# Optimization experiments

Measured on AMD Instinct MI355X. Metric: run time of the kernel, lower is better.

## Reference

```python
import jax, jax.numpy as jnp
import numpy as np
from jax import lax

B, L = 32, 128
WORD_DIM, TAG_DIM = 300, 100
EMB = WORD_DIM + TAG_DIM  # 400; LSTM hidden size == EMB
H = EMB
WV, TV = 30000, 50
MLP_H = 100


def _mk(k, shape):
    return jax.random.normal(k, shape, dtype=jnp.float32) * 0.05


def setup_inputs():
    key = jax.random.key(0)
    ks = iter(jax.random.split(key, 40))
    d = {}
    d["words_idx_tensor"] = jax.random.randint(next(ks), (B, L), 0, WV)
    d["tags_idx_tensor"] = jax.random.randint(next(ks), (B, L), 0, TV)
    d["max_length"] = L
    d["lengths"] = jax.random.randint(next(ks), (B,), 1, L + 1)
    d["word_emb"] = _mk(next(ks), (WV, WORD_DIM))
    d["tag_emb"] = _mk(next(ks), (TV, TAG_DIM))
    for name, din in (("l0", EMB), ("l0r", EMB), ("l1", 2 * H), ("l1r", 2 * H)):
        d["w_ih_" + name] = _mk(next(ks), (4 * H, din))
        d["w_hh_" + name] = _mk(next(ks), (4 * H, H))
        d["b_ih_" + name] = _mk(next(ks), (4 * H,))
        d["b_hh_" + name] = _mk(next(ks), (4 * H,))
    d["w1"] = _mk(next(ks), (MLP_H, 4 * H))
    d["b1"] = _mk(next(ks), (MLP_H,))
    d["w2"] = _mk(next(ks), (1, MLP_H))
    d["b2"] = _mk(next(ks), (1,))
    return d


def _lstm_dir(x, w_ih, w_hh, b_ih, b_hh, reverse):
    # x: (T, N, Din) time-major. PyTorch gate order: i, f, g, o.
    T, N, _ = x.shape
    xg = jnp.einsum('tnd,gd->tng', x, w_ih) + b_ih + b_hh  # (T, N, 4H)

    def step(carry, g_in):
        h, c = carry
        g = g_in + h @ w_hh.T
        i, f, gg, o = jnp.split(g, 4, axis=-1)
        c = jax.nn.sigmoid(f) * c + jax.nn.sigmoid(i) * jnp.tanh(gg)
        h = jax.nn.sigmoid(o) * jnp.tanh(c)
        return (h, c), h

    init = (jnp.zeros((N, H), x.dtype), jnp.zeros((N, H), x.dtype))
    _, hs = lax.scan(step, init, xg, reverse=reverse)
    return hs  # (T, N, H) in original time order (matches PyTorch bidir)


def _forward(words_idx, tags_idx, max_length, p):
    we = p["word_emb"][words_idx[:, :max_length]]   # (B, L, 300)
    te = p["tag_emb"][tags_idx[:, :max_length]]     # (B, L, 100)
    embeds = jnp.concatenate([we, te], axis=2)       # (B, L, 400)
    # Faithful to `embeds.view(L, B, -1)`: a RESHAPE, not a transpose.
    x = embeds.reshape(max_length, embeds.shape[0], -1)  # (L, B, 400)
    # batch_first LSTM sees batch=L, seq=B -> time-major over axis B
    h = jnp.swapaxes(x, 0, 1)                        # (B, L, 400)
    for layer in ("l0", "l1"):
        hf = _lstm_dir(h, p["w_ih_" + layer], p["w_hh_" + layer],
                       p["b_ih_" + layer], p["b_hh_" + layer], False)
        hb = _lstm_dir(h, p["w_ih_" + layer + "r"], p["w_hh_" + layer + "r"],
                       p["b_ih_" + layer + "r"], p["b_hh_" + layer + "r"], True)
        h = jnp.concatenate([hf, hb], axis=-1)       # (B, L, 2H)
    lstm_out = jnp.swapaxes(h, 0, 1)                 # (L, B, 2H)
    # Pairwise concat + Linear factorized: W1 @ [h_i; h_j] = W1a h_i + W1b h_j
    w1a, w1b = p["w1"][:, :2 * H], p["w1"][:, 2 * H:]
    a = jnp.einsum('lbd,hd->lbh', lstm_out, w1a)     # (L, B, 100)
    bm = jnp.einsum('lbd,hd->lbh', lstm_out, w1b) + p["b1"]
    hid = jnp.tanh(a[:, None] + bm[None, :])         # (L, L, B, 100)
    out = jnp.einsum('ijbh,oh->ijbo', hid, p["w2"]) + p["b2"]  # (L, L, B, 1)
    # matches torch.stack order: feature index = i * L + j
    return out.reshape(max_length * max_length, lstm_out.shape[1], 1)


def reference(words_idx_tensor, tags_idx_tensor, max_length, lengths,
              word_emb, tag_emb,
              w_ih_l0, w_hh_l0, b_ih_l0, b_hh_l0,
              w_ih_l0r, w_hh_l0r, b_ih_l0r, b_hh_l0r,
              w_ih_l1, w_hh_l1, b_ih_l1, b_hh_l1,
              w_ih_l1r, w_hh_l1r, b_ih_l1r, b_hh_l1r,
              w1, b1, w2, b2):
    p = dict(locals())
    return _forward(words_idx_tensor, tags_idx_tensor, max_length, p)
```

## Files before the change

### kernel.cpp

```cpp
#include <hip/hip_runtime.h>

typedef unsigned short u16;
typedef unsigned int u32;
typedef __attribute__((ext_vector_type(8))) short bf16x8;
typedef __attribute__((ext_vector_type(4))) float f32x4;

#define TSEQ 32
#define NB   128
#define HDIM 400
#define KPAD 416
#define G4   1600
#define TOK  4096
#define XGC  3200
#define BPITCH 420

__device__ __forceinline__ float b2f(u16 u) {
  union { unsigned int i; float f; } v; v.i = ((unsigned int)u) << 16; return v.f;
}
__device__ __forceinline__ u16 f2b(float f) {
  union { float fl; unsigned int i; } v; v.fl = f;
  unsigned int r = v.i + 0x7fffu + ((v.i >> 16) & 1u);
  return (u16)(r >> 16);
}
__device__ __forceinline__ float loadf(const void* p, long long i, int isbf) {
  return isbf ? b2f(((const u16*)p)[i]) : ((const float*)p)[i];
}
__device__ __forceinline__ u16 loadb(const void* p, long long i, int isbf) {
  return isbf ? ((const u16*)p)[i] : f2b(((const float*)p)[i]);
}
__device__ __forceinline__ float sigm_(float x) { return 1.0f / (1.0f + __expf(-x)); }
__device__ __forceinline__ float tanh_(float x) {
  float e = __expf(2.0f * x);
  return 1.0f - 2.0f / (e + 1.0f);
}

__device__ __forceinline__ void store_h16(u16* p, unsigned v) {
  asm volatile("global_store_short %0, %1, off sc0 sc1" :: "v"(p), "v"(v) : "memory");
}
__device__ __forceinline__ void store_flag(unsigned* p, unsigned v) {
  asm volatile("global_store_dword %0, %1, off sc0 sc1" :: "v"(p), "v"(v) : "memory");
}
__device__ __forceinline__ unsigned poll_cnt(const unsigned* p) {
  unsigned v;
  asm volatile("global_load_dword %0, %1, off sc0 sc1\n\ts_waitcnt vmcnt(0)"
               : "=v"(v) : "v"(p) : "memory");
  return v;
}

__global__ __launch_bounds__(256) void sniff_kernel(const void* wemb, int* flag) {
  __shared__ int cf, cb;
  if (threadIdx.x == 0) { cf = 0; cb = 0; }
  __syncthreads();
  int okf = 0, okb = 0;
  for (int i = threadIdx.x; i < 8192; i += 256) {
    float f = ((const float*)wemb)[i];
    float af = fabsf(f);
    if (af > 1e-12f && af < 8.0f) okf++;
    u16 ub = ((const u16*)wemb)[i];
    float fb = b2f(ub); float ab = fabsf(fb);
    if (ub == 0 || (ab > 1e-12f && ab < 8.0f)) okb++;
  }
  atomicAdd(&cf, okf);
  atomicAdd(&cb, okb);
  __syncthreads();
  if (threadIdx.x == 0) flag[0] = (cb > cf) ? 1 : 0;
}

__global__ __launch_bounds__(256) void embed_kernel(
    const int* __restrict__ words, const int* __restrict__ tags,
    const void* __restrict__ wemb, const void* __restrict__ temb,
    const int* __restrict__ flag, u16* __restrict__ XP) {
  const int isbf = flag[0];
  int idx = blockIdx.x * 256 + threadIdx.x;
  if (idx >= TOK * 400) return;
  int r = idx / 400, d = idx - r * 400;
  int t = r >> 7, n = r & 127;
  int m = n * 32 + t;
  int b = m >> 7, l = m & 127;
  u16 v;
  if (d < 300) v = loadb(wemb, (long long)words[b * 128 + l] * 300 + d, isbf);
  else         v = loadb(temb, (long long)tags[b * 128 + l] * 100 + (d - 300), isbf);
  XP[(size_t)r * KPAD + d] = v;
}

__global__ __launch_bounds__(256) void prep_kernel(
    const void* wih0, const void* wih1, const void* wih2, const void* wih3,
    const void* whhA0, const void* whhA1, const void* whhA2, const void* whhA3,
    const void* bih0, const void* bih1, const void* bih2, const void* bih3,
    const void* bhh0, const void* bhh1, const void* bhh2, const void* bhh3,
    const void* w1, const void* b1, const void* w2, const void* b2,
    const int* __restrict__ flag,
    u16* __restrict__ W0a, u16* __restrict__ W1a, u16* __restrict__ WhhA,
    float* __restrict__ biasA, u16* __restrict__ W1ab, float* __restrict__ smallf) {
  const int isbf = flag[0];
  long long idx = (long long)blockIdx.x * 256 + threadIdx.x;
  const void* wihs[4] = {wih0, wih1, wih2, wih3};
  const void* whhs[4] = {whhA0, whhA1, whhA2, whhA3};
  const void* bihs[4] = {bih0, bih1, bih2, bih3};
  const void* bhhs[4] = {bhh0, bhh1, bhh2, bhh3};
  const long long c1 = 1331200LL, c2 = 3891200LL, c3 = 6553600LL, c4 = 6560000LL,
                  c5 = 6726400LL, c6 = 6726601LL;
  if (idx < c1) {
    int j = (int)idx; int row = j / KPAD; int k = j - row * KPAD;
    int dir = row / G4; int ar = row - dir * G4;
    int ct = ar >> 6, rem = ar & 63, ty = rem >> 4, jj = rem & 15;
    int srow = ty * 400 + ct * 16 + jj;
    W0a[j] = (k < 400) ? loadb(wihs[dir], (long long)srow * 400 + k, isbf) : (u16)0;
  } else if (idx < c2) {
    int j = (int)(idx - c1); int row = j / 800; int k = j - row * 800;
    int dir = row / G4; int ar = row - dir * G4;
    int ct = ar >> 6, rem = ar & 63, ty = rem >> 4, jj = rem & 15;
    int srow = ty * 400 + ct * 16 + jj;
    W1a[j] = loadb(wihs[2 + dir], (long long)srow * 800 + k, isbf);
  } else if (idx < c3) {
    int j = (int)(idx - c2); int row = j / KPAD; int k = j - row * KPAD;
    int dl = row / G4; int ar = row - dl * G4;
    int ct = ar >> 6, rem = ar & 63, ty = rem >> 4, jj = rem & 15;
    int srow = ty * 400 + ct * 16 + jj;
    WhhA[j] = (k < 400) ? loadb(whhs[dl], (long long)srow * 400 + k, isbf) : (u16)0;
  } else if (idx < c4) {
    int j = (int)(idx - c3); int dl = j / G4; int ar = j - dl * G4;
    int ct = ar >> 6, rem = ar & 63, ty = rem >> 4, jj = rem & 15;
    int srow = ty * 400 + ct * 16 + jj;
    biasA[j] = loadf(bihs[dl], srow, isbf) + loadf(bhhs[dl], srow, isbf);
  } else if (idx < c5) {
    int j = (int)(idx - c4); int row = j / 800; int k = j - row * 800;
    u16 v = 0;
    if (row < 100)      v = loadb(w1, (long long)row * 1600 + k, isbf);
    else if (row < 200) v = loadb(w1, (long long)(row - 100) * 1600 + 800 + k, isbf);
    W1ab[j] = v;
  } else if (idx < c6) {
    int j = (int)(idx - c5);
    if (j < 100)       smallf[j] = loadf(b1, j, isbf);
    else if (j < 200)  smallf[j] = loadf(w2, j - 100, isbf);
    else               smallf[200] = loadf(b2, 0, isbf);
  }
}

__global__ __launch_bounds__(256) void gemm_bt(
    const u16* __restrict__ A, const u16* __restrict__ B, u16* __restrict__ C,
    int M, int N, int K) {
  __shared__ u16 As[128 * 40];
  __shared__ u16 Bs[128 * 40];
  int tid = threadIdx.x;
  int wave = tid >> 6, lane = tid & 63;
  int m0 = blockIdx.y << 7, n0 = blockIdx.x << 7;
  int wr = wave >> 1, wc = wave & 1;
  int arow = tid >> 2, aseg = tid & 3;
  const size_t aoff0 = (size_t)(m0 + arow) * K + aseg * 8;
  const size_t aoff1 = (size_t)(m0 + 64 + arow) * K + aseg * 8;
  const size_t boff0 = (size_t)(n0 + arow) * K + aseg * 8;
  const size_t boff1 = (size_t)(n0 + 64 + arow) * K + aseg * 8;
  float4 ra0 = *(const float4*)&A[aoff0];
  float4 ra1 = *(const float4*)&A[aoff1];
  float4 rb0 = *(const float4*)&B[boff0];
  float4 rb1 = *(const float4*)&B[boff1];
  f32x4 acc[4][4] = {};
  int fr = lane & 15, fkb = (lane >> 4) * 8;
  for (int k0 = 32;; k0 += 32) {
    __syncthreads();
    *(float4*)&As[arow * 40 + aseg * 8] = ra0;
    *(float4*)&As[(64 + arow) * 40 + aseg * 8] = ra1;
    *(float4*)&Bs[arow * 40 + aseg * 8] = rb0;
    *(float4*)&Bs[(64 + arow) * 40 + aseg * 8] = rb1;
    bool more = k0 < K;
    if (more) {
      ra0 = *(const float4*)&A[aoff0 + k0];
      ra1 = *(const float4*)&A[aoff1 + k0];
      rb0 = *(const float4*)&B[boff0 + k0];
      rb1 = *(const float4*)&B[boff1 + k0];
    }
    __syncthreads();
    bf16x8 af[4], bf[4];
#pragma unroll
    for (int i = 0; i < 4; i++) af[i] = *(const bf16x8*)&As[(wr * 64 + i * 16 + fr) * 40 + fkb];
#pragma unroll
    for (int i = 0; i < 4; i++) bf[i] = *(const bf16x8*)&Bs[(wc * 64 + i * 16 + fr) * 40 + fkb];
#pragma unroll
    for (int i = 0; i < 4; i++)
#pragma unroll
      for (int j = 0; j < 4; j++)
        acc[i][j] = __builtin_amdgcn_mfma_f32_16x16x32_bf16(af[i], bf[j], acc[i][j], 0, 0, 0);
    if (!more) break;
  }
  int rg = lane >> 4;
#pragma unroll
  for (int i = 0; i < 4; i++)
#pragma unroll
    for (int j = 0; j < 4; j++)
#pragma unroll
      for (int r = 0; r < 4; r++) {
        int row = m0 + wr * 64 + i * 16 + rg * 4 + r;
        int col = n0 + wc * 64 + j * 16 + fr;
        C[(size_t)row * N + col] = f2b(acc[i][j][r]);
      }
}

__global__ __launch_bounds__(256, 1) void lstm_persist(
    const u16* __restrict__ xg,
    const u16* __restrict__ Whh,
    const float* __restrict__ bias,
    u16* __restrict__ hA,
    u16* __restrict__ hB,
    u16* __restrict__ h_cat,
    unsigned* __restrict__ flags) {
  __shared__ u16 Bs[64 * BPITCH];
  __shared__ float biasS[64];
  const int ctile = blockIdx.x, ntile = blockIdx.y, dir = blockIdx.z;
  const int n0 = ntile * 64, ar0 = ctile * 64;
  const int tid = threadIdx.x, lane = tid & 63, wave = tid >> 6;
  const int fr = lane & 15, fkb = (lane >> 4) * 8, rg = lane >> 4;
  unsigned* flagbase = flags + (dir * 2 + ntile) * 32;

  const u16* wbase = Whh + ((size_t)dir * G4 + ar0) * KPAD;
  for (int idx = tid; idx < 64 * 52; idx += 256) {
    int r = idx / 52, kk = (idx - r * 52) * 8;
    *(float4*)&Bs[r * BPITCH + kk] = *(const float4*)&wbase[(size_t)r * KPAD + kk];
  }
  if (tid < 64) biasS[tid] = bias[dir * G4 + ar0 + tid];
  __syncthreads();

  const u16* hin = hA;
  u16* hout = hB;
  float c_reg[4] = {0.f, 0.f, 0.f, 0.f};
  const int cidx = ctile * 16 + fr;
  const int arow = n0 + wave * 16 + fr;
  const int erow = n0 + wave * 16 + rg * 4;

  u16 xv[16];
  {
    const int t0 = dir ? 31 : 0;
    const u16* xcol = xg + (size_t)t0 * 128 * XGC + (size_t)dir * G4 + ar0 + fr;
#pragma unroll
    for (int r = 0; r < 4; r++) {
      const u16* p = xcol + (size_t)(erow + r) * XGC;
      xv[r * 4 + 0] = p[0];  xv[r * 4 + 1] = p[16];
      xv[r * 4 + 2] = p[32]; xv[r * 4 + 3] = p[48];
    }
  }

  for (int s = 0; s < TSEQ; s++) {
    const int t = dir ? (31 - s) : s;
    f32x4 acc[4] = {};
    if (s > 0) {
      if (tid < 25) {
        const unsigned tgt = (unsigned)s;
        while (poll_cnt(&flagbase[tid]) < tgt) __builtin_amdgcn_s_sleep(2);
      }
      __syncthreads();
      const u16* hb = hin + ((size_t)dir * NB + arow) * KPAD + fkb;
      bf16x8 areg[13];
#pragma unroll
      for (int k = 0; k < 13; k++) {
        const u16* p = hb + k * 32;
        asm volatile("global_load_dwordx4 %0, %1, off sc0 sc1" : "=v"(areg[k]) : "v"(p));
      }
      asm volatile("s_waitcnt vmcnt(0)" ::: "memory");
      __builtin_amdgcn_sched_barrier(0);
#pragma unroll
      for (int k = 0; k < 13; k++) {
#pragma unroll
        for (int j = 0; j < 4; j++) {
          bf16x8 b = *(const bf16x8*)&Bs[(j * 16 + fr) * BPITCH + k * 32 + fkb];
          acc[j] = __builtin_amdgcn_mfma_f32_16x16x32_bf16(areg[k], b, acc[j], 0, 0, 0);
        }
      }
    }
    u16 hvals[4];
#pragma unroll
    for (int r = 0; r < 4; r++) {
      float gi = acc[0][r] + b2f(xv[r * 4 + 0]) + biasS[fr];
      float gf = acc[1][r] + b2f(xv[r * 4 + 1]) + biasS[16 + fr];
      float gg = acc[2][r] + b2f(xv[r * 4 + 2]) + biasS[32 + fr];
      float go = acc[3][r] + b2f(xv[r * 4 + 3]) + biasS[48 + fr];
      float c_new = sigm_(gf) * c_reg[r] + sigm_(gi) * tanh_(gg);
      float h_new = sigm_(go) * tanh_(c_new);
      c_reg[r] = c_new;
      hvals[r] = f2b(h_new);
      store_h16(&hout[((size_t)dir * NB + erow + r) * KPAD + cidx], (unsigned)hvals[r]);
    }
    asm volatile("s_waitcnt vmcnt(0)" ::: "memory");
    __syncthreads();
    if (tid == 0) store_flag(&flagbase[ctile], (unsigned)(s + 1));
#pragma unroll
    for (int r = 0; r < 4; r++)
      h_cat[(size_t)(t * 128 + erow + r) * 800 + dir * HDIM + cidx] = hvals[r];
    {
      const int sn = (s < 31) ? (s + 1) : 31;
      const int tn = dir ? (31 - sn) : sn;
      const u16* xcol = xg + (size_t)tn * 128 * XGC + (size_t)dir * G4 + ar0 + fr;
#pragma unroll
      for (int r = 0; r < 4; r++) {
        const u16* p = xcol + (size_t)(erow + r) * XGC;
        xv[r * 4 + 0] = p[0];  xv[r * 4 + 1] = p[16];
        xv[r * 4 + 2] = p[32]; xv[r * 4 + 3] = p[48];
      }
    }
    u16* tmp = (u16*)hin; hin = hout; hout = tmp;
  }
}

__global__ __launch_bounds__(256) void ab_gemm(
    const u16* __restrict__ h1, const u16* __restrict__ W1ab,
    const float* __restrict__ smallf, float* __restrict__ abuf, float* __restrict__ bbuf) {
  int lane = threadIdx.x & 63, wv = threadIdx.x >> 6;
  int mt = blockIdx.y * 4 + wv;
  int nt = blockIdx.x;
  int r0 = mt * 16, c0 = nt * 16;
  f32x4 acc = {};
  int fr = lane & 15, fk8 = (lane >> 4) * 8;
  for (int k0 = 0; k0 < 800; k0 += 32) {
    bf16x8 a = *(const bf16x8*)&h1[(size_t)(r0 + fr) * 800 + k0 + fk8];
    bf16x8 b = *(const bf16x8*)&W1ab[(size_t)(c0 + fr) * 800 + k0 + fk8];
    acc = __builtin_amdgcn_mfma_f32_16x16x32_bf16(a, b, acc, 0, 0, 0);
  }
  int c = c0 + fr;
  if (c < 200) {
#pragma unroll
    for (int r = 0; r < 4; r++) {
      int row = r0 + (lane >> 4) * 4 + r;
      int t = row >> 7, n = row & 127;
      int orow = n * 32 + t;
      float v = acc[r];
      if (c < 100) abuf[(size_t)orow * 100 + c] = v;
      else         bbuf[(size_t)orow * 100 + (c - 100)] = v + smallf[c - 100];
    }
  }
}

__global__ __launch_bounds__(256) void pairwise(
    const float* __restrict__ abuf, const float* __restrict__ bbuf,
    const float* __restrict__ smallf, const int* __restrict__ flag,
    void* __restrict__ outp) {
  __shared__ float aS[16 * 101];
  __shared__ float bS[16 * 101];
  __shared__ float w2S[104];
  int b = blockIdx.z, i0 = blockIdx.y * 16, j0 = blockIdx.x * 16;
  int tid = threadIdx.x;
  for (int idx = tid; idx < 1600; idx += 256) {
    int r = idx / 100, h = idx - r * 100;
    aS[r * 101 + h] = abuf[((size_t)(i0 + r) * 32 + b) * 100 + h];
    bS[r * 101 + h] = bbuf[((size_t)(j0 + r) * 32 + b) * 100 + h];
  }
  if (tid < 100) w2S[tid] = smallf[100 + tid];
  __syncthreads();
  float bias2 = smallf[200];
  int di = tid >> 4, dj = tid & 15;
  const float* ar = &aS[di * 101];
  const float* br = &bS[dj * 101];
  float s = 0.0f;
#pragma unroll 4
  for (int h = 0; h < 100; h++) s += w2S[h] * tanh_(ar[h] + br[h]);
  int i = i0 + di, j = j0 + dj;
  size_t pos = ((size_t)(i * 128 + j)) * 32 + b;
  float v = s + bias2;
  if (flag[0]) ((u16*)outp)[pos] = f2b(v);
  else         ((float*)outp)[pos] = v;
}

extern "C" void kernel_launch(void* const* d_in, const int* in_sizes, int n_in,
                              void* d_out, int out_size, void* d_ws, size_t ws_size,
                              hipStream_t stream) {
  (void)in_sizes; (void)n_in; (void)out_size; (void)ws_size;
  const int* words = (const int*)d_in[0];
  const int* tags  = (const int*)d_in[1];
  const void* wemb = d_in[4];
  const void* temb = d_in[5];
  const void* wih[4] = {d_in[6],  d_in[10], d_in[14], d_in[18]};
  const void* whh[4] = {d_in[7],  d_in[11], d_in[15], d_in[19]};
  const void* bih[4] = {d_in[8],  d_in[12], d_in[16], d_in[20]};
  const void* bhh[4] = {d_in[9],  d_in[13], d_in[17], d_in[21]};
  const void* w1 = d_in[22];
  const void* b1 = d_in[23];
  const void* w2 = d_in[24];
  const void* b2 = d_in[25];

  char* ws = (char*)d_ws;
  size_t off = 0;
  auto alloc = [&](size_t bytes) -> void* {
    void* p = ws + off; off = (off + bytes + 255) & ~(size_t)255; return p;
  };
  int*      flag  = (int*)     alloc(256);
  u16*      hstate= (u16*)     alloc((size_t)2 * 2 * NB * KPAD * 2);
  unsigned* flags = (unsigned*)alloc(1024);
  float*    smallf= (float*)   alloc(201 * 4);
  float*    abuf  = (float*)   alloc((size_t)TOK * 100 * 4);
  float*    bbuf  = (float*)   alloc((size_t)TOK * 100 * 4);
  u16*      hcat0 = (u16*)     alloc((size_t)TOK * 800 * 2);
  u16*      hcat1 = (u16*)     alloc((size_t)TOK * 800 * 2);
  u16*      XP    = (u16*)     alloc((size_t)TOK * KPAD * 2);
  u16*      xg    = (u16*)     alloc((size_t)TOK * XGC * 2);
  u16*      W0a   = (u16*)     alloc((size_t)2 * G4 * KPAD * 2);
  u16*      W1a   = (u16*)     alloc((size_t)2 * G4 * 800 * 2);
  u16*      WhhA  = (u16*)     alloc((size_t)4 * G4 * KPAD * 2);
  float*    biasA = (float*)   alloc((size_t)4 * G4 * 4);
  u16*      W1ab  = (u16*)     alloc((size_t)208 * 800 * 2);

  u16* h0 = hstate;
  u16* h1 = hstate + (size_t)2 * NB * KPAD;

  sniff_kernel<<<1, 256, 0, stream>>>(wemb, flag);
  hipMemsetAsync(flags, 0, 1024, stream);
  prep_kernel<<<26276, 256, 0, stream>>>(
      wih[0], wih[1], wih[2], wih[3], whh[0], whh[1], whh[2], whh[3],
      bih[0], bih[1], bih[2], bih[3], bhh[0], bhh[1], bhh[2], bhh[3],
      w1, b1, w2, b2, flag, W0a, W1a, WhhA, biasA, W1ab, smallf);
  embed_kernel<<<6400, 256, 0, stream>>>(words, tags, wemb, temb, flag, XP);

  gemm_bt<<<dim3(25, 32), 256, 0, stream>>>(XP, W0a, xg, TOK, XGC, KPAD);
  lstm_persist<<<dim3(25, 2, 2), 256, 0, stream>>>(
      xg, WhhA, biasA, h0, h1, hcat0, flags);

  gemm_bt<<<dim3(25, 32), 256, 0, stream>>>(hcat0, W1a, xg, TOK, XGC, 800);
  lstm_persist<<<dim3(25, 2, 2), 256, 0, stream>>>(
      xg, WhhA + (size_t)2 * G4 * KPAD, biasA + 2 * G4, h0, h1, hcat1, flags + 128);

  ab_gemm<<<dim3(13, 64), 256, 0, stream>>>(hcat1, W1ab, smallf, abuf, bbuf);
  pairwise<<<dim3(8, 8, 32), 256, 0, stream>>>(abuf, bbuf, smallf, flag, d_out);
}
```

Baseline: 435.4 us.

## Fuse input projection GEMM into persistent LSTM and drop dtype sniffing

Removes the separate input-projection GEMM and its large xg intermediate buffer. Each persistent LSTM block now computes its own x·W_ih slice with MFMA for the next timestep, right after publishing h, so this work overlaps the recurrent wait. It also drops the bf16/fp32 sniff kernel, hard-codes fp32 inputs and outputs, and merges the embedding gather into the prep kernel. The cost is extra MFMA and global weight reads inside the serial recurrence loop, and the input dtype is no longer detected at run time.

```diff
diff --git a/kernel.cpp b/kernel.cpp
--- a/kernel.cpp
+++ b/kernel.cpp
@@ -11,7 +11,6 @@
 #define KPAD 416
 #define G4   1600
 #define TOK  4096
-#define XGC  3200
 #define BPITCH 420
 
 __device__ __forceinline__ float b2f(u16 u) {
@@ -21,12 +20,6 @@
   union { float fl; unsigned int i; } v; v.fl = f;
   unsigned int r = v.i + 0x7fffu + ((v.i >> 16) & 1u);
   return (u16)(r >> 16);
-}
-__device__ __forceinline__ float loadf(const void* p, long long i, int isbf) {
-  return isbf ? b2f(((const u16*)p)[i]) : ((const float*)p)[i];
-}
-__device__ __forceinline__ u16 loadb(const void* p, long long i, int isbf) {
-  return isbf ? ((const u16*)p)[i] : f2b(((const float*)p)[i]);
 }
 __device__ __forceinline__ float sigm_(float x) { return 1.0f / (1.0f + __expf(-x)); }
 __device__ __forceinline__ float tanh_(float x) {
@@ -47,163 +40,82 @@
   return v;
 }
 
-__global__ __launch_bounds__(256) void sniff_kernel(const void* wemb, int* flag) {
-  __shared__ int cf, cb;
-  if (threadIdx.x == 0) { cf = 0; cb = 0; }
-  __syncthreads();
-  int okf = 0, okb = 0;
-  for (int i = threadIdx.x; i < 8192; i += 256) {
-    float f = ((const float*)wemb)[i];
-    float af = fabsf(f);
-    if (af > 1e-12f && af < 8.0f) okf++;
-    u16 ub = ((const u16*)wemb)[i];
-    float fb = b2f(ub); float ab = fabsf(fb);
-    if (ub == 0 || (ab > 1e-12f && ab < 8.0f)) okb++;
-  }
-  atomicAdd(&cf, okf);
-  atomicAdd(&cb, okb);
-  __syncthreads();
-  if (threadIdx.x == 0) flag[0] = (cb > cf) ? 1 : 0;
-}
-
-__global__ __launch_bounds__(256) void embed_kernel(
+__global__ __launch_bounds__(256) void prep_embed(
+    const float* wih0, const float* wih1, const float* wih2, const float* wih3,
+    const float* whhA0, const float* whhA1, const float* whhA2, const float* whhA3,
+    const float* bih0, const float* bih1, const float* bih2, const float* bih3,
+    const float* bhh0, const float* bhh1, const float* bhh2, const float* bhh3,
+    const float* w1, const float* b1, const float* w2, const float* b2,
     const int* __restrict__ words, const int* __restrict__ tags,
-    const void* __restrict__ wemb, const void* __restrict__ temb,
-    const int* __restrict__ flag, u16* __restrict__ XP) {
-  const int isbf = flag[0];
-  int idx = blockIdx.x * 256 + threadIdx.x;
-  if (idx >= TOK * 400) return;
-  int r = idx / 400, d = idx - r * 400;
-  int t = r >> 7, n = r & 127;
-  int m = n * 32 + t;
-  int b = m >> 7, l = m & 127;
-  u16 v;
-  if (d < 300) v = loadb(wemb, (long long)words[b * 128 + l] * 300 + d, isbf);
-  else         v = loadb(temb, (long long)tags[b * 128 + l] * 100 + (d - 300), isbf);
-  XP[(size_t)r * KPAD + d] = v;
-}
-
-__global__ __launch_bounds__(256) void prep_kernel(
-    const void* wih0, const void* wih1, const void* wih2, const void* wih3,
-    const void* whhA0, const void* whhA1, const void* whhA2, const void* whhA3,
-    const void* bih0, const void* bih1, const void* bih2, const void* bih3,
-    const void* bhh0, const void* bhh1, const void* bhh2, const void* bhh3,
-    const void* w1, const void* b1, const void* w2, const void* b2,
-    const int* __restrict__ flag,
+    const float* __restrict__ wemb, const float* __restrict__ temb,
     u16* __restrict__ W0a, u16* __restrict__ W1a, u16* __restrict__ WhhA,
-    float* __restrict__ biasA, u16* __restrict__ W1ab, float* __restrict__ smallf) {
-  const int isbf = flag[0];
+    float* __restrict__ biasA, u16* __restrict__ W1ab, float* __restrict__ smallf,
+    u16* __restrict__ XP) {
   long long idx = (long long)blockIdx.x * 256 + threadIdx.x;
-  const void* wihs[4] = {wih0, wih1, wih2, wih3};
-  const void* whhs[4] = {whhA0, whhA1, whhA2, whhA3};
-  const void* bihs[4] = {bih0, bih1, bih2, bih3};
-  const void* bhhs[4] = {bhh0, bhh1, bhh2, bhh3};
+  const float* wihs[4] = {wih0, wih1, wih2, wih3};
+  const float* whhs[4] = {whhA0, whhA1, whhA2, whhA3};
+  const float* bihs[4] = {bih0, bih1, bih2, bih3};
+  const float* bhhs[4] = {bhh0, bhh1, bhh2, bhh3};
   const long long c1 = 1331200LL, c2 = 3891200LL, c3 = 6553600LL, c4 = 6560000LL,
-                  c5 = 6726400LL, c6 = 6726601LL;
+                  c5 = 6726400LL, c6 = 6726601LL, c7 = 8365001LL;
   if (idx < c1) {
     int j = (int)idx; int row = j / KPAD; int k = j - row * KPAD;
     int dir = row / G4; int ar = row - dir * G4;
     int ct = ar >> 6, rem = ar & 63, ty = rem >> 4, jj = rem & 15;
     int srow = ty * 400 + ct * 16 + jj;
-    W0a[j] = (k < 400) ? loadb(wihs[dir], (long long)srow * 400 + k, isbf) : (u16)0;
+    W0a[j] = (k < 400) ? f2b(wihs[dir][(size_t)srow * 400 + k]) : (u16)0;
   } else if (idx < c2) {
     int j = (int)(idx - c1); int row = j / 800; int k = j - row * 800;
     int dir = row / G4; int ar = row - dir * G4;
     int ct = ar >> 6, rem = ar & 63, ty = rem >> 4, jj = rem & 15;
     int srow = ty * 400 + ct * 16 + jj;
-    W1a[j] = loadb(wihs[2 + dir], (long long)srow * 800 + k, isbf);
+    W1a[j] = f2b(wihs[2 + dir][(size_t)srow * 800 + k]);
   } else if (idx < c3) {
     int j = (int)(idx - c2); int row = j / KPAD; int k = j - row * KPAD;
     int dl = row / G4; int ar = row - dl * G4;
     int ct = ar >> 6, rem = ar & 63, ty = rem >> 4, jj = rem & 15;
     int srow = ty * 400 + ct * 16 + jj;
-    WhhA[j] = (k < 400) ? loadb(whhs[dl], (long long)srow * 400 + k, isbf) : (u16)0;
+    WhhA[j] = (k < 400) ? f2b(whhs[dl][(size_t)srow * 400 + k]) : (u16)0;
   } else if (idx < c4) {
     int j = (int)(idx - c3); int dl = j / G4; int ar = j - dl * G4;
     int ct = ar >> 6, rem = ar & 63, ty = rem >> 4, jj = rem & 15;
     int srow = ty * 400 + ct * 16 + jj;
-    biasA[j] = loadf(bihs[dl], srow, isbf) + loadf(bhhs[dl], srow, isbf);
+    biasA[j] = bihs[dl][srow] + bhhs[dl][srow];
   } else if (idx < c5) {
     int j = (int)(idx - c4); int row = j / 800; int k = j - row * 800;
     u16 v = 0;
-    if (row < 100)      v = loadb(w1, (long long)row * 1600 + k, isbf);
-    else if (row < 200) v = loadb(w1, (long long)(row - 100) * 1600 + 800 + k, isbf);
+    if (row < 100)      v = f2b(w1[(size_t)row * 1600 + k]);
+    else if (row < 200) v = f2b(w1[(size_t)(row - 100) * 1600 + 800 + k]);
     W1ab[j] = v;
   } else if (idx < c6) {
     int j = (int)(idx - c5);
-    if (j < 100)       smallf[j] = loadf(b1, j, isbf);
-    else if (j < 200)  smallf[j] = loadf(w2, j - 100, isbf);
-    else               smallf[200] = loadf(b2, 0, isbf);
-  }
-}
-
-__global__ __launch_bounds__(256) void gemm_bt(
-    const u16* __restrict__ A, const u16* __restrict__ B, u16* __restrict__ C,
-    int M, int N, int K) {
-  __shared__ u16 As[128 * 40];
-  __shared__ u16 Bs[128 * 40];
-  int tid = threadIdx.x;
-  int wave = tid >> 6, lane = tid & 63;
-  int m0 = blockIdx.y << 7, n0 = blockIdx.x << 7;
-  int wr = wave >> 1, wc = wave & 1;
-  int arow = tid >> 2, aseg = tid & 3;
-  const size_t aoff0 = (size_t)(m0 + arow) * K + aseg * 8;
-  const size_t aoff1 = (size_t)(m0 + 64 + arow) * K + aseg * 8;
-  const size_t boff0 = (size_t)(n0 + arow) * K + aseg * 8;
-  const size_t boff1 = (size_t)(n0 + 64 + arow) * K + aseg * 8;
-  float4 ra0 = *(const float4*)&A[aoff0];
-  float4 ra1 = *(const float4*)&A[aoff1];
-  float4 rb0 = *(const float4*)&B[boff0];
-  float4 rb1 = *(const float4*)&B[boff1];
-  f32x4 acc[4][4] = {};
-  int fr = lane & 15, fkb = (lane >> 4) * 8;
-  for (int k0 = 32;; k0 += 32) {
-    __syncthreads();
-    *(float4*)&As[arow * 40 + aseg * 8] = ra0;
-    *(float4*)&As[(64 + arow) * 40 + aseg * 8] = ra1;
-    *(float4*)&Bs[arow * 40 + aseg * 8] = rb0;
-    *(float4*)&Bs[(64 + arow) * 40 + aseg * 8] = rb1;
-    bool more = k0 < K;
-    if (more) {
-      ra0 = *(const float4*)&A[aoff0 + k0];
-      ra1 = *(const float4*)&A[aoff1 + k0];
-      rb0 = *(const float4*)&B[boff0 + k0];
-      rb1 = *(const float4*)&B[boff1 + k0];
-    }
-    __syncthreads();
-    bf16x8 af[4], bf[4];
-#pragma unroll
-    for (int i = 0; i < 4; i++) af[i] = *(const bf16x8*)&As[(wr * 64 + i * 16 + fr) * 40 + fkb];
-#pragma unroll
-    for (int i = 0; i < 4; i++) bf[i] = *(const bf16x8*)&Bs[(wc * 64 + i * 16 + fr) * 40 + fkb];
-#pragma unroll
-    for (int i = 0; i < 4; i++)
-#pragma unroll
-      for (int j = 0; j < 4; j++)
-        acc[i][j] = __builtin_amdgcn_mfma_f32_16x16x32_bf16(af[i], bf[j], acc[i][j], 0, 0, 0);
-    if (!more) break;
-  }
-  int rg = lane >> 4;
-#pragma unroll
-  for (int i = 0; i < 4; i++)
-#pragma unroll
-    for (int j = 0; j < 4; j++)
-#pragma unroll
-      for (int r = 0; r < 4; r++) {
-        int row = m0 + wr * 64 + i * 16 + rg * 4 + r;
-        int col = n0 + wc * 64 + j * 16 + fr;
-        C[(size_t)row * N + col] = f2b(acc[i][j][r]);
-      }
-}
-
+    if (j < 100)       smallf[j] = b1[j];
+    else if (j < 200)  smallf[j] = w2[j - 100];
+    else               smallf[200] = b2[0];
+  } else if (idx < c7) {
+    int j = (int)(idx - c6);
+    int r = j / 400, d = j - r * 400;
+    int t = r >> 7, n = r & 127;
+    int m = n * 32 + t;
+    int b = m >> 7, l = m & 127;
+    u16 v;
+    if (d < 300) v = f2b(wemb[(size_t)words[b * 128 + l] * 300 + d]);
+    else         v = f2b(temb[(size_t)tags[b * 128 + l] * 100 + (d - 300)]);
+    XP[(size_t)r * KPAD + d] = v;
+  }
+}
+
+template<int XK>
 __global__ __launch_bounds__(256, 1) void lstm_persist(
-    const u16* __restrict__ xg,
+    const u16* __restrict__ X,
+    const u16* __restrict__ Wih,
     const u16* __restrict__ Whh,
     const float* __restrict__ bias,
     u16* __restrict__ hA,
     u16* __restrict__ hB,
     u16* __restrict__ h_cat,
     unsigned* __restrict__ flags) {
+  constexpr int KX = XK / 32;
   __shared__ u16 Bs[64 * BPITCH];
   __shared__ float biasS[64];
   const int ctile = blockIdx.x, ntile = blockIdx.y, dir = blockIdx.z;
@@ -226,22 +138,25 @@
   const int cidx = ctile * 16 + fr;
   const int arow = n0 + wave * 16 + fr;
   const int erow = n0 + wave * 16 + rg * 4;
-
-  u16 xv[16];
+  const u16* wib = Wih + ((size_t)dir * G4 + ar0) * XK;
+
+  f32x4 accC[4] = {};
   {
     const int t0 = dir ? 31 : 0;
-    const u16* xcol = xg + (size_t)t0 * 128 * XGC + (size_t)dir * G4 + ar0 + fr;
-#pragma unroll
-    for (int r = 0; r < 4; r++) {
-      const u16* p = xcol + (size_t)(erow + r) * XGC;
-      xv[r * 4 + 0] = p[0];  xv[r * 4 + 1] = p[16];
-      xv[r * 4 + 2] = p[32]; xv[r * 4 + 3] = p[48];
+    const u16* xr = X + ((size_t)(t0 * 128) + arow) * XK + fkb;
+#pragma unroll
+    for (int k = 0; k < KX; k++) {
+      bf16x8 a = *(const bf16x8*)&xr[k * 32];
+#pragma unroll
+      for (int j = 0; j < 4; j++) {
+        bf16x8 b = *(const bf16x8*)&wib[(size_t)(j * 16 + fr) * XK + k * 32 + fkb];
+        accC[j] = __builtin_amdgcn_mfma_f32_16x16x32_bf16(a, b, accC[j], 0, 0, 0);
+      }
     }
   }
 
   for (int s = 0; s < TSEQ; s++) {
     const int t = dir ? (31 - s) : s;
-    f32x4 acc[4] = {};
     if (s > 0) {
       if (tid < 25) {
         const unsigned tgt = (unsigned)s;
@@ -258,21 +173,20 @@
       asm volatile("s_waitcnt vmcnt(0)" ::: "memory");
       __builtin_amdgcn_sched_barrier(0);
 #pragma unroll
-      for (int k = 0; k < 13; k++) {
+      for (int k = 0; k < 13; k++)
 #pragma unroll
         for (int j = 0; j < 4; j++) {
           bf16x8 b = *(const bf16x8*)&Bs[(j * 16 + fr) * BPITCH + k * 32 + fkb];
-          acc[j] = __builtin_amdgcn_mfma_f32_16x16x32_bf16(areg[k], b, acc[j], 0, 0, 0);
+          accC[j] = __builtin_amdgcn_mfma_f32_16x16x32_bf16(areg[k], b, accC[j], 0, 0, 0);
         }
-      }
     }
     u16 hvals[4];
 #pragma unroll
     for (int r = 0; r < 4; r++) {
-      float gi = acc[0][r] + b2f(xv[r * 4 + 0]) + biasS[fr];
-      float gf = acc[1][r] + b2f(xv[r * 4 + 1]) + biasS[16 + fr];
-      float gg = acc[2][r] + b2f(xv[r * 4 + 2]) + biasS[32 + fr];
-      float go = acc[3][r] + b2f(xv[r * 4 + 3]) + biasS[48 + fr];
+      float gi = accC[0][r] + biasS[fr];
+      float gf = accC[1][r] + biasS[16 + fr];
+      float gg = accC[2][r] + biasS[32 + fr];
+      float go = accC[3][r] + biasS[48 + fr];
       float c_new = sigm_(gf) * c_reg[r] + sigm_(gi) * tanh_(gg);
       float h_new = sigm_(go) * tanh_(c_new);
       c_reg[r] = c_new;
@@ -285,17 +199,22 @@
 #pragma unroll
     for (int r = 0; r < 4; r++)
       h_cat[(size_t)(t * 128 + erow + r) * 800 + dir * HDIM + cidx] = hvals[r];
-    {
-      const int sn = (s < 31) ? (s + 1) : 31;
-      const int tn = dir ? (31 - sn) : sn;
-      const u16* xcol = xg + (size_t)tn * 128 * XGC + (size_t)dir * G4 + ar0 + fr;
-#pragma unroll
-      for (int r = 0; r < 4; r++) {
-        const u16* p = xcol + (size_t)(erow + r) * XGC;
-        xv[r * 4 + 0] = p[0];  xv[r * 4 + 1] = p[16];
-        xv[r * 4 + 2] = p[32]; xv[r * 4 + 3] = p[48];
+    f32x4 accN[4] = {};
+    if (s < 31) {
+      const int tn = dir ? (31 - (s + 1)) : (s + 1);
+      const u16* xr = X + ((size_t)(tn * 128) + arow) * XK + fkb;
+#pragma unroll
+      for (int k = 0; k < KX; k++) {
+        bf16x8 a = *(const bf16x8*)&xr[k * 32];
+#pragma unroll
+        for (int j = 0; j < 4; j++) {
+          bf16x8 b = *(const bf16x8*)&wib[(size_t)(j * 16 + fr) * XK + k * 32 + fkb];
+          accN[j] = __builtin_amdgcn_mfma_f32_16x16x32_bf16(a, b, accN[j], 0, 0, 0);
+        }
       }
     }
+#pragma unroll
+    for (int j = 0; j < 4; j++) accC[j] = accN[j];
     u16* tmp = (u16*)hin; hin = hout; hout = tmp;
   }
 }
@@ -330,8 +249,7 @@
 
 __global__ __launch_bounds__(256) void pairwise(
     const float* __restrict__ abuf, const float* __restrict__ bbuf,
-    const float* __restrict__ smallf, const int* __restrict__ flag,
-    void* __restrict__ outp) {
+    const float* __restrict__ smallf, float* __restrict__ outp) {
   __shared__ float aS[16 * 101];
   __shared__ float bS[16 * 101];
   __shared__ float w2S[104];
@@ -352,10 +270,7 @@
 #pragma unroll 4
   for (int h = 0; h < 100; h++) s += w2S[h] * tanh_(ar[h] + br[h]);
   int i = i0 + di, j = j0 + dj;
-  size_t pos = ((size_t)(i * 128 + j)) * 32 + b;
-  float v = s + bias2;
-  if (flag[0]) ((u16*)outp)[pos] = f2b(v);
-  else         ((float*)outp)[pos] = v;
+  outp[((size_t)(i * 128 + j)) * 32 + b] = s + bias2;
 }
 
 extern "C" void kernel_launch(void* const* d_in, const int* in_sizes, int n_in,
@@ -364,23 +279,27 @@
   (void)in_sizes; (void)n_in; (void)out_size; (void)ws_size;
   const int* words = (const int*)d_in[0];
   const int* tags  = (const int*)d_in[1];
-  const void* wemb = d_in[4];
-  const void* temb = d_in[5];
-  const void* wih[4] = {d_in[6],  d_in[10], d_in[14], d_in[18]};
-  const void* whh[4] = {d_in[7],  d_in[11], d_in[15], d_in[19]};
-  const void* bih[4] = {d_in[8],  d_in[12], d_in[16], d_in[20]};
-  const void* bhh[4] = {d_in[9],  d_in[13], d_in[17], d_in[21]};
-  const void* w1 = d_in[22];
-  const void* b1 = d_in[23];
-  const void* w2 = d_in[24];
-  const void* b2 = d_in[25];
+  const float* wemb = (const float*)d_in[4];
+  const float* temb = (const float*)d_in[5];
+  const float* wih[4] = {(const float*)d_in[6],  (const float*)d_in[10],
+                         (const float*)d_in[14], (const float*)d_in[18]};
+  const float* whh[4] = {(const float*)d_in[7],  (const float*)d_in[11],
+                         (const float*)d_in[15], (const float*)d_in[19]};
+  const float* bih[4] = {(const float*)d_in[8],  (const float*)d_in[12],
+                         (const float*)d_in[16], (const float*)d_in[20]};
+  const float* bhh[4] = {(const float*)d_in[9],  (const float*)d_in[13],
+                         (const float*)d_in[17], (const float*)d_in[21]};
+  const float* w1 = (const float*)d_in[22];
+  const float* b1 = (const float*)d_in[23];
+  const float* w2 = (const float*)d_in[24];
+  const float* b2 = (const float*)d_in[25];
+  float* out = (float*)d_out;
 
   char* ws = (char*)d_ws;
   size_t off = 0;
   auto alloc = [&](size_t bytes) -> void* {
     void* p = ws + off; off = (off + bytes + 255) & ~(size_t)255; return p;
   };
-  int*      flag  = (int*)     alloc(256);
   u16*      hstate= (u16*)     alloc((size_t)2 * 2 * NB * KPAD * 2);
   unsigned* flags = (unsigned*)alloc(1024);
   float*    smallf= (float*)   alloc(201 * 4);
@@ -389,7 +308,6 @@
   u16*      hcat0 = (u16*)     alloc((size_t)TOK * 800 * 2);
   u16*      hcat1 = (u16*)     alloc((size_t)TOK * 800 * 2);
   u16*      XP    = (u16*)     alloc((size_t)TOK * KPAD * 2);
-  u16*      xg    = (u16*)     alloc((size_t)TOK * XGC * 2);
   u16*      W0a   = (u16*)     alloc((size_t)2 * G4 * KPAD * 2);
   u16*      W1a   = (u16*)     alloc((size_t)2 * G4 * 800 * 2);
   u16*      WhhA  = (u16*)     alloc((size_t)4 * G4 * KPAD * 2);
@@ -399,22 +317,20 @@
   u16* h0 = hstate;
   u16* h1 = hstate + (size_t)2 * NB * KPAD;
 
-  sniff_kernel<<<1, 256, 0, stream>>>(wemb, flag);
-  hipMemsetAsync(flags, 0, 1024, stream);
-  prep_kernel<<<26276, 256, 0, stream>>>(
+  (void)hipMemsetAsync(flags, 0, 1024, stream);
+  prep_embed<<<32677, 256, 0, stream>>>(
       wih[0], wih[1], wih[2], wih[3], whh[0], whh[1], whh[2], whh[3],
       bih[0], bih[1], bih[2], bih[3], bhh[0], bhh[1], bhh[2], bhh[3],
-      w1, b1, w2, b2, flag, W0a, W1a, WhhA, biasA, W1ab, smallf);
-  embed_kernel<<<6400, 256, 0, stream>>>(words, tags, wemb, temb, flag, XP);
-
-  gemm_bt<<<dim3(25, 32), 256, 0, stream>>>(XP, W0a, xg, TOK, XGC, KPAD);
-  lstm_persist<<<dim3(25, 2, 2), 256, 0, stream>>>(
-      xg, WhhA, biasA, h0, h1, hcat0, flags);
-
-  gemm_bt<<<dim3(25, 32), 256, 0, stream>>>(hcat0, W1a, xg, TOK, XGC, 800);
-  lstm_persist<<<dim3(25, 2, 2), 256, 0, stream>>>(
-      xg, WhhA + (size_t)2 * G4 * KPAD, biasA + 2 * G4, h0, h1, hcat1, flags + 128);
+      w1, b1, w2, b2, words, tags, wemb, temb,
+      W0a, W1a, WhhA, biasA, W1ab, smallf, XP);
+
+  lstm_persist<KPAD><<<dim3(25, 2, 2), 256, 0, stream>>>(
+      XP, W0a, WhhA, biasA, h0, h1, hcat0, flags);
+
+  lstm_persist<800><<<dim3(25, 2, 2), 256, 0, stream>>>(
+      hcat0, W1a, WhhA + (size_t)2 * G4 * KPAD, biasA + 2 * G4,
+      h0, h1, hcat1, flags + 128);
 
   ab_gemm<<<dim3(13, 64), 256, 0, stream>>>(hcat1, W1ab, smallf, abuf, bbuf);
-  pairwise<<<dim3(8, 8, 32), 256, 0, stream>>>(abuf, bbuf, smallf, flag, d_out);
-}
+  pairwise<<<dim3(8, 8, 32), 256, 0, stream>>>(abuf, bbuf, smallf, out);
+}
```

Result: slower. 882.4 us (+102.6%).
